# Kernel tuning notes

Measured on AMD Instinct MI355X. Metric: run time of the kernel, lower is better.

## Reference

```python
import jax, jax.numpy as jnp
import numpy as np

N, E, F_IN, H1, H2, C = 100000, 800000, 182, 128, 64, 2


def setup_inputs() -> dict:
    key = jax.random.key(0)
    ks = jax.random.split(key, 10)
    s = 0.05
    return {
        "x": jax.random.normal(ks[0], (N, F_IN), dtype=jnp.float32),
        "edge_index": jax.random.randint(ks[1], (2, E), 0, N, dtype=jnp.int32),
        "W1_l": jax.random.normal(ks[2], (H1, F_IN), dtype=jnp.float32) * s,
        "W1_r": jax.random.normal(ks[3], (H1, F_IN), dtype=jnp.float32) * s,
        "b1": jnp.zeros((H1,), dtype=jnp.float32),
        "W2_l": jax.random.normal(ks[4], (H2, H1), dtype=jnp.float32) * s,
        "W2_r": jax.random.normal(ks[5], (H2, H1), dtype=jnp.float32) * s,
        "b2": jnp.zeros((H2,), dtype=jnp.float32),
        "W_lin": jax.random.normal(ks[6], (C, H2), dtype=jnp.float32) * s,
        "b_lin": jnp.zeros((C,), dtype=jnp.float32),
    }


def _sage_conv(x, src, dst, Wl, Wr, b):
    # mean-aggregate neighbor messages x[src] onto dst, then two linears
    msg = x[src]                                            # [E, F]
    ssum = jax.ops.segment_sum(msg, dst, num_segments=N)    # [N, F]
    cnt = jax.ops.segment_sum(jnp.ones((src.shape[0], 1), x.dtype), dst, num_segments=N)
    mean = ssum / jnp.maximum(cnt, 1.0)                     # [N, F]
    return mean @ Wl.T + x @ Wr.T + b                       # [N, F_out]


def reference(x, edge_index, W1_l, W1_r, b1, W2_l, W2_r, b2, W_lin, b_lin):
    src, dst = edge_index[0], edge_index[1]
    h = jax.nn.relu(_sage_conv(x, src, dst, W1_l, W1_r, b1))   # dropout is identity in eval
    h = jax.nn.relu(_sage_conv(h, src, dst, W2_l, W2_r, b2))
    logits = h @ W_lin.T + b_lin
    return jax.nn.log_softmax(logits, axis=1)
```

## Files before the change

kernel.cpp:

```cpp
#include <hip/hip_runtime.h>
#include <hip/hip_bf16.h>
#include <math.h>

#define F_IN 182
#define H1   128
#define H2   64
#define CAPS 6

typedef short bf16x8 __attribute__((ext_vector_type(8)));
typedef float f32x4 __attribute__((ext_vector_type(4)));

__device__ __forceinline__ float b2f(short s) {
    unsigned u = ((unsigned)(unsigned short)s) << 16;
    return __builtin_bit_cast(float, u);
}
__device__ __forceinline__ short f2b(float f) {
    return __builtin_bit_cast(short, __float2bfloat16(f));
}
__device__ __forceinline__ short2 f2x2(float2 f) {
    short2 r;
    r.x = f2b(f.x);
    r.y = f2b(f.y);
    return r;
}

#define GLOAD16(g, l) __builtin_amdgcn_global_load_lds( \
    (const __attribute__((address_space(1))) void*)(g), \
    (__attribute__((address_space(3))) void*)(l), 16, 0, 0)

__global__ __launch_bounds__(256) void prelude(
    int* __restrict__ cnt, int Nn, int zB,
    const float* __restrict__ W1l, const float* __restrict__ W1r, short* __restrict__ wc1,
    const float* __restrict__ W2l, const float* __restrict__ W2r, short* __restrict__ wc2)
{
    int b = blockIdx.x, tid = threadIdx.x;
    if (b < zB) {
        int i = (b * 256 + tid) * 4;
        if (i + 4 <= Nn) {
            int4 z = make_int4(0, 0, 0, 0);
            *(int4*)(cnt + i) = z;
        } else {
            for (int j = i; j < Nn; ++j) cnt[j] = 0;
        }
        return;
    }
    b -= zB;
    if (b < 192) {
        int idx = b * 256 + tid;
        int r = idx / 192, k = idx - r * 192;
        float v = 0.f;
        if (k < F_IN) v = (r < 128) ? W1l[r * F_IN + k] : W1r[(r - 128) * F_IN + k];
        wc1[idx] = f2b(v);
        return;
    }
    b -= 192;
    {
        int idx = b * 256 + tid;
        int r = idx >> 7, k = idx & 127;
        float v = (r < 64) ? W2l[r * 128 + k] : W2r[(r - 64) * 128 + k];
        wc2[idx] = f2b(v);
    }
}

template <int NC, int KK, int KREAL, bool DEG>
__global__ __launch_bounds__(512) void gemm_fused(
    const void* __restrict__ Ap, const short* __restrict__ Wcat,
    short* __restrict__ outL, short* __restrict__ outR, int M,
    const int* __restrict__ srcv, const int* __restrict__ dstv,
    int* __restrict__ cnt, int* __restrict__ csr_pad,
    int E, int degB)
{
    constexpr int BM = 128, BK = 64;
    constexpr int WN = NC / 4;
    constexpr int NJ = WN / 16;
    constexpr int CB = NC * 8 / 512;
    __shared__ __attribute__((aligned(16))) short sA[BM * BK];
    __shared__ __attribute__((aligned(16))) short sB[NC * BK];
    int tid = threadIdx.x;

    if (DEG && (int)blockIdx.x < degB) {
        int tstep = degB * 512 * 4;
        int gtid = (int)blockIdx.x * 512 + tid;
        for (int base = gtid * 4; base + 4 <= E; base += tstep) {
            int4 d = *(const int4*)(dstv + base);
            int4 s = *(const int4*)(srcv + base);
            int p0 = atomicAdd(&cnt[d.x], 1);
            int p1 = atomicAdd(&cnt[d.y], 1);
            int p2 = atomicAdd(&cnt[d.z], 1);
            int p3 = atomicAdd(&cnt[d.w], 1);
            if (p0 < (1 << CAPS)) csr_pad[((size_t)d.x << CAPS) + p0] = s.x;
            if (p1 < (1 << CAPS)) csr_pad[((size_t)d.y << CAPS) + p1] = s.y;
            if (p2 < (1 << CAPS)) csr_pad[((size_t)d.z << CAPS) + p2] = s.z;
            if (p3 < (1 << CAPS)) csr_pad[((size_t)d.w << CAPS) + p3] = s.w;
        }
        if (gtid == 0) {
            for (int e = E & ~3; e < E; ++e) {
                int p = atomicAdd(&cnt[dstv[e]], 1);
                if (p < (1 << CAPS)) csr_pad[((size_t)dstv[e] << CAPS) + p] = srcv[e];
            }
        }
        return;
    }
    int bx = DEG ? ((int)blockIdx.x - degB) : (int)blockIdx.x;
    int wid = tid >> 6, lane = tid & 63;
    int wr = wid >> 2, wc = wid & 3;
    int row0 = bx * BM;
    f32x4 acc[4][NJ] = {};
#pragma unroll
    for (int ksi = 0; ksi < KK / BK; ++ksi) {
        const int k0 = ksi * BK;
        {
            const float* Af = (const float*)Ap;
#pragma unroll
            for (int it = 0; it < 2; ++it) {
                int i = it * 512 + tid;
                int r = i >> 3, oct = i & 7;
                int gr = row0 + r;
                int gk = k0 + oct * 8;
                bf16x8 v = {};
                if (gr < M) {
                    const float* p = Af + (size_t)gr * KREAL + gk;
                    if (k0 + BK <= KREAL) {
                        float2 f0 = *(const float2*)(p + 0);
                        float2 f1 = *(const float2*)(p + 2);
                        float2 f2 = *(const float2*)(p + 4);
                        float2 f3 = *(const float2*)(p + 6);
                        short2 p0 = f2x2(f0), p1 = f2x2(f1), p2 = f2x2(f2), p3 = f2x2(f3);
                        v[0] = p0.x; v[1] = p0.y; v[2] = p1.x; v[3] = p1.y;
                        v[4] = p2.x; v[5] = p2.y; v[6] = p3.x; v[7] = p3.y;
                    } else {
#pragma unroll
                        for (int j = 0; j < 4; ++j) {
                            if (gk + 2 * j + 2 <= KREAL) {
                                short2 pj = f2x2(*(const float2*)(p + 2 * j));
                                v[2 * j] = pj.x; v[2 * j + 1] = pj.y;
                            }
                        }
                    }
                }
                *(bf16x8*)((char*)sA + r * 128 + ((oct * 16) ^ ((r & 7) << 4))) = v;
            }
        }
#pragma unroll
        for (int c = 0; c < CB; ++c) {
            int idx = (wid * CB + c) * 64 + lane;
            int r = idx >> 3, cs = (idx & 7) * 16;
            const char* g = (const char*)Wcat + (size_t)r * (KK * 2) + k0 * 2 + (cs ^ ((r & 7) << 4));
            GLOAD16(g, (char*)sB + (size_t)(wid * CB + c) * 1024);
        }
        __syncthreads();
        int rl = lane & 15;
        int sw = (rl & 7) << 4;
#pragma unroll
        for (int ks = 0; ks < 2; ++ks) {
            int kb2 = ks * 64 + (lane >> 4) * 16;
            int cswz = kb2 ^ sw;
            bf16x8 af[4];
#pragma unroll
            for (int mi = 0; mi < 4; ++mi) {
                int row = wr * 64 + mi * 16 + rl;
                af[mi] = *(const bf16x8*)((const char*)sA + row * 128 + cswz);
            }
#pragma unroll
            for (int ni = 0; ni < NJ; ++ni) {
                int rowb = wc * WN + ni * 16 + rl;
                bf16x8 bfr = *(const bf16x8*)((const char*)sB + rowb * 128 + cswz);
#pragma unroll
                for (int mi = 0; mi < 4; ++mi)
                    acc[mi][ni] = __builtin_amdgcn_mfma_f32_16x16x32_bf16(af[mi], bfr, acc[mi][ni], 0, 0, 0);
            }
        }
        __syncthreads();
    }
    constexpr int HN = NC / 2;
#pragma unroll
    for (int mi = 0; mi < 4; ++mi) {
#pragma unroll
        for (int ni = 0; ni < NJ; ++ni) {
            int gc = wc * WN + ni * 16 + (lane & 15);
#pragma unroll
            for (int r = 0; r < 4; ++r) {
                int gr = row0 + wr * 64 + mi * 16 + (lane >> 4) * 4 + r;
                if (gr < M) {
                    short v = f2b(acc[mi][ni][r]);
                    if (gc < HN) outL[(size_t)gr * HN + gc] = v;
                    else         outR[(size_t)gr * HN + gc - HN] = v;
                }
            }
        }
    }
}

__global__ __launch_bounds__(512) void agg_gemm2(
    const int* __restrict__ degs, const int* __restrict__ csr_pad,
    const short* __restrict__ y1l, const short* __restrict__ y1r,
    const float* __restrict__ b1, const short* __restrict__ wc2,
    short* __restrict__ outL, short* __restrict__ outR, int M)
{
    constexpr int BM = 128, NC = 128;
    constexpr int WN = NC / 4;
    constexpr int NJ = WN / 16;
    __shared__ __attribute__((aligned(16))) short sA[BM * 128];
    __shared__ __attribute__((aligned(16))) short sB[NC * 128];
    int tid = threadIdx.x;
    int wid = tid >> 6, lane = tid & 63;
    int wr = wid >> 2, wc = wid & 3;
    int row0 = (int)blockIdx.x * BM;

#pragma unroll
    for (int it = 0; it < 4; ++it) {
        int idx = (wid * 4 + it) * 64 + lane;
        int r = idx >> 4, c16 = (idx & 15) * 16;
        const char* g = (const char*)wc2 + (size_t)r * 256 + (c16 ^ ((r & 7) << 4));
        GLOAD16(g, (char*)sB + (size_t)(wid * 4 + it) * 1024);
    }

    int rlocal = tid >> 4;
    int l = tid & 15;
    const int co = l * 8;
#pragma unroll
    for (int rr = 0; rr < 4; ++rr) {
        int r = rr * 32 + rlocal;
        int gid = row0 + r;
        bf16x8 o = {};
        if (gid < M) {
            const int* crow = csr_pad + ((size_t)gid << CAPS);
            int deg = degs[gid];
            float a[8] = {};
            int t = 0;
            for (; t + 8 <= deg; t += 8) {
                int idx[8];
#pragma unroll
                for (int q = 0; q < 8; ++q) idx[q] = crow[t + q];
                bf16x8 vv[8];
#pragma unroll
                for (int q = 0; q < 8; ++q) vv[q] = *(const bf16x8*)(y1l + (size_t)idx[q] * H1 + co);
#pragma unroll
                for (int j = 0; j < 8; ++j) {
                    float s = 0.f;
#pragma unroll
                    for (int q = 0; q < 8; ++q) s += b2f(vv[q][j]);
                    a[j] += s;
                }
            }
            for (; t + 4 <= deg; t += 4) {
                int i0 = crow[t], i1 = crow[t + 1];
                int i2 = crow[t + 2], i3 = crow[t + 3];
                bf16x8 v0 = *(const bf16x8*)(y1l + (size_t)i0 * H1 + co);
                bf16x8 v1 = *(const bf16x8*)(y1l + (size_t)i1 * H1 + co);
                bf16x8 v2 = *(const bf16x8*)(y1l + (size_t)i2 * H1 + co);
                bf16x8 v3 = *(const bf16x8*)(y1l + (size_t)i3 * H1 + co);
#pragma unroll
                for (int j = 0; j < 8; ++j)
                    a[j] += b2f(v0[j]) + b2f(v1[j]) + b2f(v2[j]) + b2f(v3[j]);
            }
            for (; t < deg; ++t) {
                int s = crow[t];
                bf16x8 v = *(const bf16x8*)(y1l + (size_t)s * H1 + co);
#pragma unroll
                for (int j = 0; j < 8; ++j) a[j] += b2f(v[j]);
            }
            float inv = 1.f / fmaxf((float)deg, 1.f);
            bf16x8 rv = *(const bf16x8*)(y1r + (size_t)gid * H1 + co);
#pragma unroll
            for (int j = 0; j < 8; ++j)
                o[j] = f2b(fmaxf(a[j] * inv + b2f(rv[j]) + b1[co + j], 0.f));
        }
        *(bf16x8*)((char*)sA + r * 256 + ((co * 2) ^ ((r & 7) << 4))) = o;
    }
    __syncthreads();

    f32x4 acc[4][NJ] = {};
    int rl = lane & 15;
    int sw = (rl & 7) << 4;
#pragma unroll
    for (int ks = 0; ks < 4; ++ks) {
        int kcol = (ks * 4 + (lane >> 4)) * 16;
        int cswz = kcol ^ sw;
        bf16x8 af[4];
#pragma unroll
        for (int mi = 0; mi < 4; ++mi) {
            int row = wr * 64 + mi * 16 + rl;
            af[mi] = *(const bf16x8*)((const char*)sA + row * 256 + cswz);
        }
#pragma unroll
        for (int ni = 0; ni < NJ; ++ni) {
            int rowb = wc * WN + ni * 16 + rl;
            bf16x8 bfr = *(const bf16x8*)((const char*)sB + rowb * 256 + cswz);
#pragma unroll
            for (int mi = 0; mi < 4; ++mi)
                acc[mi][ni] = __builtin_amdgcn_mfma_f32_16x16x32_bf16(af[mi], bfr, acc[mi][ni], 0, 0, 0);
        }
    }
    constexpr int HN = NC / 2;
#pragma unroll
    for (int mi = 0; mi < 4; ++mi) {
#pragma unroll
        for (int ni = 0; ni < NJ; ++ni) {
            int gc = wc * WN + ni * 16 + (lane & 15);
#pragma unroll
            for (int r = 0; r < 4; ++r) {
                int gr = row0 + wr * 64 + mi * 16 + (lane >> 4) * 4 + r;
                if (gr < M) {
                    short v = f2b(acc[mi][ni][r]);
                    if (gc < HN) outL[(size_t)gr * HN + gc] = v;
                    else         outR[(size_t)gr * HN + gc - HN] = v;
                }
            }
        }
    }
}

__global__ __launch_bounds__(256) void agg_head2(const int* __restrict__ degs,
                                                 const int* __restrict__ csr_pad,
                                                 const short* __restrict__ yl,
                                                 const short* __restrict__ yr,
                                                 const float* __restrict__ bias,
                                                 const float* __restrict__ Wlin,
                                                 const float* __restrict__ blin,
                                                 float* __restrict__ out, int Nn) {
    int gid = blockIdx.x * 16 + (threadIdx.x >> 4);
    int l = threadIdx.x & 15;
    if (gid >= Nn) return;
    const int* crow = csr_pad + ((size_t)gid << CAPS);
    int deg = degs[gid];
    const int co = l * 4;
    float a[4] = {};
    int t = 0;
    for (; t + 8 <= deg; t += 8) {
        int idx[8];
#pragma unroll
        for (int q = 0; q < 8; ++q) idx[q] = crow[t + q];
        short4 vv[8];
#pragma unroll
        for (int q = 0; q < 8; ++q) vv[q] = *(const short4*)(yl + (size_t)idx[q] * H2 + co);
#pragma unroll
        for (int q = 0; q < 8; ++q) {
            a[0] += b2f(vv[q].x); a[1] += b2f(vv[q].y);
            a[2] += b2f(vv[q].z); a[3] += b2f(vv[q].w);
        }
    }
    for (; t + 4 <= deg; t += 4) {
        int i0 = crow[t], i1 = crow[t + 1];
        int i2 = crow[t + 2], i3 = crow[t + 3];
        short4 v0 = *(const short4*)(yl + (size_t)i0 * H2 + co);
        short4 v1 = *(const short4*)(yl + (size_t)i1 * H2 + co);
        short4 v2 = *(const short4*)(yl + (size_t)i2 * H2 + co);
        short4 v3 = *(const short4*)(yl + (size_t)i3 * H2 + co);
        a[0] += b2f(v0.x) + b2f(v1.x) + b2f(v2.x) + b2f(v3.x);
        a[1] += b2f(v0.y) + b2f(v1.y) + b2f(v2.y) + b2f(v3.y);
        a[2] += b2f(v0.z) + b2f(v1.z) + b2f(v2.z) + b2f(v3.z);
        a[3] += b2f(v0.w) + b2f(v1.w) + b2f(v2.w) + b2f(v3.w);
    }
    for (; t < deg; ++t) {
        int s = crow[t];
        short4 v = *(const short4*)(yl + (size_t)s * H2 + co);
        a[0] += b2f(v.x); a[1] += b2f(v.y); a[2] += b2f(v.z); a[3] += b2f(v.w);
    }
    float inv = 1.f / fmaxf((float)deg, 1.f);
    short4 rv = *(const short4*)(yr + (size_t)gid * H2 + co);
    float h0 = fmaxf(a[0] * inv + b2f(rv.x) + bias[co + 0], 0.f);
    float h1v = fmaxf(a[1] * inv + b2f(rv.y) + bias[co + 1], 0.f);
    float h2v = fmaxf(a[2] * inv + b2f(rv.z) + bias[co + 2], 0.f);
    float h3v = fmaxf(a[3] * inv + b2f(rv.w) + bias[co + 3], 0.f);
    float g0 = h0 * Wlin[co] + h1v * Wlin[co + 1] + h2v * Wlin[co + 2] + h3v * Wlin[co + 3];
    float g1 = h0 * Wlin[64 + co] + h1v * Wlin[64 + co + 1] + h2v * Wlin[64 + co + 2] + h3v * Wlin[64 + co + 3];
#pragma unroll
    for (int m = 8; m >= 1; m >>= 1) {
        g0 += __shfl_xor(g0, m, 16);
        g1 += __shfl_xor(g1, m, 16);
    }
    if (l == 0) {
        g0 += blin[0]; g1 += blin[1];
        float mx = fmaxf(g0, g1);
        float lse = mx + logf(expf(g0 - mx) + expf(g1 - mx));
        float2 r; r.x = g0 - lse; r.y = g1 - lse;
        ((float2*)out)[gid] = r;
    }
}

extern "C" void kernel_launch(void* const* d_in, const int* in_sizes, int n_in,
                              void* d_out, int out_size, void* d_ws, size_t ws_size,
                              hipStream_t stream) {
    const float* x    = (const float*)d_in[0];
    const int*   ei   = (const int*)d_in[1];
    const float* W1l  = (const float*)d_in[2];
    const float* W1r  = (const float*)d_in[3];
    const float* b1   = (const float*)d_in[4];
    const float* W2l  = (const float*)d_in[5];
    const float* W2r  = (const float*)d_in[6];
    const float* b2   = (const float*)d_in[7];
    const float* Wlin = (const float*)d_in[8];
    const float* blin = (const float*)d_in[9];
    float* outp = (float*)d_out;

    const int N = in_sizes[0] / F_IN;
    const int E = in_sizes[1] / 2;
    const int* srcv = ei;
    const int* dstv = ei + E;

    char* ws = (char*)d_ws;
    size_t o = 0;
    auto alloc = [&](size_t bytes) { size_t r = o; o += (bytes + 255) & ~(size_t)255; return r; };
    int* cnt_i   = (int*)(ws + alloc((size_t)N * 4));
    int* csr_pad = (int*)(ws + alloc(((size_t)N << CAPS) * 4));
    short* wc1   = (short*)(ws + alloc((size_t)256 * 192 * 2));
    short* wc2   = (short*)(ws + alloc((size_t)128 * 128 * 2));
    short* y1l   = (short*)(ws + alloc((size_t)N * H1 * 2));
    short* y1r   = (short*)(ws + alloc((size_t)N * H1 * 2));
    short* y2l   = (short*)(ws + alloc((size_t)N * H2 * 2));
    short* y2r   = (short*)(ws + alloc((size_t)N * H2 * 2));

    const int zB   = (N + 1023) / 1024;
    const int degB = 64;
    const int gblk = (N + 127) / 128;
    const int a16  = (N + 15) / 16;

    prelude<<<zB + 192 + 64, 256, 0, stream>>>(cnt_i, N, zB, W1l, W1r, wc1, W2l, W2r, wc2);

    gemm_fused<256, 192, F_IN, true><<<degB + gblk, 512, 0, stream>>>(
        x, wc1, y1l, y1r, N, srcv, dstv, cnt_i, csr_pad, E, degB);

    agg_gemm2<<<gblk, 512, 0, stream>>>(cnt_i, csr_pad, y1l, y1r, b1, wc2, y2l, y2r, N);

    agg_head2<<<a16, 256, 0, stream>>>(cnt_i, csr_pad, y2l, y2r, b2, Wlin, blin, outp, N);
}
```

Measured before the change: 144.3 us.

## Split CSR build into atomic rank pass and separate scatter kernel

The degree-count blocks fused into the layer-1 GEMM now only perform the atomic increments and store each edge's rank to a new buffer, without reading src or writing into the padded CSR. A new kernel then scatters src indices into the padded CSR using the stored ranks. The aim is to shorten the serial dependency chain inside the blocks that share time with the GEMM, so they finish sooner. The cost is an extra launch plus an E-sized rank buffer that is written and then read back.

After: 147.2 us. +2.0%, slower.

```diff
diff --git a/kernel.cpp b/kernel.cpp
--- a/kernel.cpp
+++ b/kernel.cpp
@@ -62,12 +62,39 @@
     }
 }
 
+__global__ __launch_bounds__(256) void csr_scatter_pad(const int* __restrict__ srcv,
+                                                       const int* __restrict__ dstv,
+                                                       const int* __restrict__ rank,
+                                                       int* __restrict__ csr_pad, int E) {
+    int base = (blockIdx.x * 256 + threadIdx.x) * 8;
+    if (base + 8 <= E) {
+        int4 d0 = *(const int4*)(dstv + base);
+        int4 d1 = *(const int4*)(dstv + base + 4);
+        int4 s0 = *(const int4*)(srcv + base);
+        int4 s1 = *(const int4*)(srcv + base + 4);
+        int4 r0 = *(const int4*)(rank + base);
+        int4 r1 = *(const int4*)(rank + base + 4);
+        if (r0.x < (1 << CAPS)) csr_pad[((size_t)d0.x << CAPS) + r0.x] = s0.x;
+        if (r0.y < (1 << CAPS)) csr_pad[((size_t)d0.y << CAPS) + r0.y] = s0.y;
+        if (r0.z < (1 << CAPS)) csr_pad[((size_t)d0.z << CAPS) + r0.z] = s0.z;
+        if (r0.w < (1 << CAPS)) csr_pad[((size_t)d0.w << CAPS) + r0.w] = s0.w;
+        if (r1.x < (1 << CAPS)) csr_pad[((size_t)d1.x << CAPS) + r1.x] = s1.x;
+        if (r1.y < (1 << CAPS)) csr_pad[((size_t)d1.y << CAPS) + r1.y] = s1.y;
+        if (r1.z < (1 << CAPS)) csr_pad[((size_t)d1.z << CAPS) + r1.z] = s1.z;
+        if (r1.w < (1 << CAPS)) csr_pad[((size_t)d1.w << CAPS) + r1.w] = s1.w;
+    } else {
+        for (int e = base; e < E; ++e) {
+            int r = rank[e];
+            if (r < (1 << CAPS)) csr_pad[((size_t)dstv[e] << CAPS) + r] = srcv[e];
+        }
+    }
+}
+
 template <int NC, int KK, int KREAL, bool DEG>
 __global__ __launch_bounds__(512) void gemm_fused(
     const void* __restrict__ Ap, const short* __restrict__ Wcat,
     short* __restrict__ outL, short* __restrict__ outR, int M,
-    const int* __restrict__ srcv, const int* __restrict__ dstv,
-    int* __restrict__ cnt, int* __restrict__ csr_pad,
+    const int* __restrict__ dstv, int* __restrict__ cnt, int* __restrict__ rank,
     int E, int degB)
 {
     constexpr int BM = 128, BK = 64;
@@ -83,21 +110,15 @@
         int gtid = (int)blockIdx.x * 512 + tid;
         for (int base = gtid * 4; base + 4 <= E; base += tstep) {
             int4 d = *(const int4*)(dstv + base);
-            int4 s = *(const int4*)(srcv + base);
-            int p0 = atomicAdd(&cnt[d.x], 1);
-            int p1 = atomicAdd(&cnt[d.y], 1);
-            int p2 = atomicAdd(&cnt[d.z], 1);
-            int p3 = atomicAdd(&cnt[d.w], 1);
-            if (p0 < (1 << CAPS)) csr_pad[((size_t)d.x << CAPS) + p0] = s.x;
-            if (p1 < (1 << CAPS)) csr_pad[((size_t)d.y << CAPS) + p1] = s.y;
-            if (p2 < (1 << CAPS)) csr_pad[((size_t)d.z << CAPS) + p2] = s.z;
-            if (p3 < (1 << CAPS)) csr_pad[((size_t)d.w << CAPS) + p3] = s.w;
+            int4 rk;
+            rk.x = atomicAdd(&cnt[d.x], 1);
+            rk.y = atomicAdd(&cnt[d.y], 1);
+            rk.z = atomicAdd(&cnt[d.z], 1);
+            rk.w = atomicAdd(&cnt[d.w], 1);
+            *(int4*)(rank + base) = rk;
         }
         if (gtid == 0) {
-            for (int e = E & ~3; e < E; ++e) {
-                int p = atomicAdd(&cnt[dstv[e]], 1);
-                if (p < (1 << CAPS)) csr_pad[((size_t)dstv[e] << CAPS) + p] = srcv[e];
-            }
+            for (int e = E & ~3; e < E; ++e) rank[e] = atomicAdd(&cnt[dstv[e]], 1);
         }
         return;
     }
@@ -403,6 +424,7 @@
     size_t o = 0;
     auto alloc = [&](size_t bytes) { size_t r = o; o += (bytes + 255) & ~(size_t)255; return r; };
     int* cnt_i   = (int*)(ws + alloc((size_t)N * 4));
+    int* rank    = (int*)(ws + alloc((size_t)E * 4));
     int* csr_pad = (int*)(ws + alloc(((size_t)N << CAPS) * 4));
     short* wc1   = (short*)(ws + alloc((size_t)256 * 192 * 2));
     short* wc2   = (short*)(ws + alloc((size_t)128 * 128 * 2));
@@ -414,12 +436,15 @@
     const int zB   = (N + 1023) / 1024;
     const int degB = 64;
     const int gblk = (N + 127) / 128;
+    const int e8   = (E + 2047) / 2048;
     const int a16  = (N + 15) / 16;
 
     prelude<<<zB + 192 + 64, 256, 0, stream>>>(cnt_i, N, zB, W1l, W1r, wc1, W2l, W2r, wc2);
 
     gemm_fused<256, 192, F_IN, true><<<degB + gblk, 512, 0, stream>>>(
-        x, wc1, y1l, y1r, N, srcv, dstv, cnt_i, csr_pad, E, degB);
+        x, wc1, y1l, y1r, N, dstv, cnt_i, rank, E, degB);
+
+    csr_scatter_pad<<<e8, 256, 0, stream>>>(srcv, dstv, rank, csr_pad, E);
 
     agg_gemm2<<<gblk, 512, 0, stream>>>(cnt_i, csr_pad, y1l, y1r, b1, wc2, y2l, y2r, N);
 
```
